# Kernel tuning notes

Hardware: AMD Instinct MI355X
Metric: run time of the kernel (lower is better)

Reference implementation:

```python
import jax, jax.numpy as jnp
import numpy as np

H, KVH, D = 32, 8, 128          # heads, kv heads, head dim
WINDOW = 512                     # sliding_window
NEG = -1e30


def _rotate_half(x):
    x1, x2 = jnp.split(x, 2, axis=-1)
    return jnp.concatenate([-x2, x1], axis=-1)


def setup_inputs() -> dict:
    key = jax.random.key(0)
    ks = jax.random.split(key, 6)
    B, S = 4, 1024
    T = B * S
    hidden = H * D  # 4096
    # RoPE tables [max_pos, head_dim]
    inv_freq = 1.0 / (10000.0 ** (jnp.arange(0, D, 2, dtype=jnp.float32) / D))
    freqs = jnp.outer(jnp.arange(S, dtype=jnp.float32), inv_freq)
    emb = jnp.concatenate([freqs, freqs], axis=-1)
    cos, sin = jnp.cos(emb), jnp.sin(emb)
    x = jax.random.normal(ks[0], (T, hidden), dtype=jnp.float32)
    pos = jnp.tile(jnp.arange(S, dtype=jnp.int64), B)            # positions restart per seq
    cu = jnp.arange(B + 1, dtype=jnp.int32) * S                  # uniform varlen offsets
    sc = 0.02
    Wq = jax.random.normal(ks[1], (hidden, H * D), jnp.float32) * sc
    Wk = jax.random.normal(ks[2], (hidden, KVH * D), jnp.float32) * sc
    Wv = jax.random.normal(ks[3], (hidden, KVH * D), jnp.float32) * sc
    Wo = jax.random.normal(ks[4], (H * D, hidden), jnp.float32) * sc
    return {"cos": cos, "sin": sin, "nz_hidden_states": x,
            "nz_position_ids": pos, "cu_seqlens": cu, "max_seqlen": S,
            "Wq": Wq, "Wk": Wk, "Wv": Wv, "Wo": Wo}


def reference(cos, sin, nz_hidden_states, nz_position_ids, cu_seqlens, max_seqlen,
              Wq, Wk, Wv, Wo):
    T = nz_hidden_states.shape[0]
    q = (nz_hidden_states @ Wq).reshape(T, H, D)
    k = (nz_hidden_states @ Wk).reshape(T, KVH, D)
    v = (nz_hidden_states @ Wv).reshape(T, KVH, D)
    # RoPE: gather by position, broadcast over head dim (unsqueeze(-2))
    c = cos[nz_position_ids][:, None, :]
    s = sin[nz_position_ids][:, None, :]
    q = q * c + _rotate_half(q) * s
    k = k * c + _rotate_half(k) * s
    # uniform varlen -> batch view [B, S, ...]
    B = cu_seqlens.shape[0] - 1
    S = T // B
    G = H // KVH  # query heads per kv head (GQA)
    qb = q.reshape(B, S, KVH, G, D)
    kb = k.reshape(B, S, KVH, D)
    vb = v.reshape(B, S, KVH, D)
    scores = jnp.einsum('bqhgd,bkhd->bhgqk', qb, kb) / jnp.sqrt(jnp.float32(D))
    i = jnp.arange(S)[:, None]
    j = jnp.arange(S)[None, :]
    mask = (j <= i) & (i - j <= WINDOW)  # causal + sliding window
    scores = jnp.where(mask, scores, NEG)
    p = jax.nn.softmax(scores, axis=-1)
    out = jnp.einsum('bhgqk,bkhd->bqhgd', p, vb).reshape(T, H * D)
    return out @ Wo
```

## Files before the change

### kernel.cpp

```cpp
#include <hip/hip_runtime.h>

typedef __bf16 bf16_t;
typedef __bf16 bf16x8 __attribute__((ext_vector_type(8)));
typedef __bf16 bf16x4 __attribute__((ext_vector_type(4)));
typedef float  f32x4  __attribute__((ext_vector_type(4)));
typedef float  f32x16 __attribute__((ext_vector_type(16)));
typedef unsigned int u32x4 __attribute__((ext_vector_type(4)));

#define N_HEADS 32
#define N_KVH   8
#define HEADDIM 128
#define WINDOW  512
#define NBATCH  4
#define SEQLEN  1024
#define NTOK    (NBATCH * SEQLEN)
#define HIDDEN  4096
#define QKVW    6144

__device__ __forceinline__ void llds16(const bf16_t* g, const bf16_t* l)
{
    __builtin_amdgcn_global_load_lds(
        (const __attribute__((address_space(1))) void*)g,
        (__attribute__((address_space(3))) void*)l, 16, 0, 0);
}

template<bool OUT_F32>
__global__ __launch_bounds__(512, 2)
void gemm256_kernel(const bf16_t* __restrict__ A, const bf16_t* __restrict__ Bt,
                    void* __restrict__ Cp, int M, int N, int K)
{
    __shared__ __align__(16) char lds[4 * 32768];
    const int tid  = threadIdx.x;
    const int w    = tid >> 6, lane = tid & 63;
    const int ntx  = N >> 8;
    const int nwg  = gridDim.x;
    const int cpx  = nwg >> 3;
    const int lin  = blockIdx.x;
    const int swz  = (nwg & 7) == 0 ? (lin & 7) * cpx + (lin >> 3) : lin;
    const int m0   = (swz / ntx) * 256;
    const int n0   = (swz % ntx) * 256;
    const int wm   = (w >> 2) * 128;
    const int wn   = (w & 3) * 64;
    const int fr   = lane & 15;
    const int kslot16 = (((lane >> 4) ^ ((lane >> 1) & 3)) << 4);
    const int srcblk  = (((tid & 3) ^ ((tid >> 3) & 3)) << 3);
    const int nk = K >> 5;

    f32x4 acc[8][4];
#pragma unroll
    for (int i = 0; i < 8; ++i)
#pragma unroll
        for (int j = 0; j < 4; ++j) {
            acc[i][j][0] = 0.f; acc[i][j][1] = 0.f;
            acc[i][j][2] = 0.f; acc[i][j][3] = 0.f;
        }

    const bf16_t* arow = A  + (size_t)(m0 + (tid >> 2)) * K + srcblk;
    const bf16_t* brow = Bt + (size_t)(n0 + (tid >> 2)) * K + srcblk;
    const size_t rowK128 = (size_t)128 * K;

    auto STAGE = [&](int tt) {
        char* dst = lds + (tt & 3) * 32768 + w * 1024;
        const int kt = tt << 5;
#pragma unroll
        for (int j = 0; j < 2; ++j)
            llds16(arow + j * rowK128 + kt, (const bf16_t*)(dst + j * 8192));
#pragma unroll
        for (int j = 0; j < 2; ++j)
            llds16(brow + j * rowK128 + kt, (const bf16_t*)(dst + 16384 + j * 8192));
    };

    STAGE(0); STAGE(1); STAGE(2);

    for (int t = 0; t < nk; ++t) {
        if (t < nk - 2)       asm volatile("s_waitcnt vmcnt(8)" ::: "memory");
        else if (t == nk - 2) asm volatile("s_waitcnt vmcnt(4)" ::: "memory");
        else                  asm volatile("s_waitcnt vmcnt(0)" ::: "memory");
        __builtin_amdgcn_sched_barrier(0);
        __builtin_amdgcn_s_barrier();
        __builtin_amdgcn_sched_barrier(0);

        const char* base = lds + (t & 3) * 32768;
        bf16x8 af[8], bfg[4];
#pragma unroll
        for (int mt = 0; mt < 8; ++mt)
            af[mt] = *(const bf16x8*)(base + ((wm + mt * 16 + fr) << 6) + kslot16);
#pragma unroll
        for (int nt = 0; nt < 4; ++nt)
            bfg[nt] = *(const bf16x8*)(base + 16384 + ((wn + nt * 16 + fr) << 6) + kslot16);

        if (t + 3 < nk) STAGE(t + 3);
        __builtin_amdgcn_s_setprio(1);
#pragma unroll
        for (int mt = 0; mt < 8; ++mt)
#pragma unroll
            for (int nt = 0; nt < 4; ++nt)
                acc[mt][nt] = __builtin_amdgcn_mfma_f32_16x16x32_bf16(
                    af[mt], bfg[nt], acc[mt][nt], 0, 0, 0);
        __builtin_amdgcn_s_setprio(0);
    }

    const int r0 = (lane >> 4) << 2;
#pragma unroll
    for (int mt = 0; mt < 8; ++mt)
#pragma unroll
        for (int nt = 0; nt < 4; ++nt)
#pragma unroll
            for (int r = 0; r < 4; ++r) {
                int row = m0 + wm + mt * 16 + r0 + r;
                int col = n0 + wn + nt * 16 + fr;
                if constexpr (OUT_F32)
                    ((float*)Cp)[(size_t)row * N + col] = acc[mt][nt][r];
                else
                    ((bf16_t*)Cp)[(size_t)row * N + col] = (bf16_t)acc[mt][nt][r];
            }
}

template<bool A_F32, bool OUT_F32>
__global__ __launch_bounds__(256)
void gemm_kernel(const void* __restrict__ Ap, const void* __restrict__ Bp,
                 void* __restrict__ Cp, int M, int N, int K)
{
    __shared__ bf16_t As[128 * 40];
    __shared__ bf16_t Bs[128 * 40];
    const int tid  = threadIdx.x;
    const int m0   = blockIdx.y * 128;
    const int n0   = blockIdx.x * 128;
    const int wave = tid >> 6, lane = tid & 63;
    const int wm   = (wave >> 1) * 64, wn = (wave & 1) * 64;
    const int fr   = lane & 15;
    const int koff = (lane >> 4) * 8;

    f32x4 acc[4][4];
#pragma unroll
    for (int i = 0; i < 4; ++i)
#pragma unroll
        for (int j = 0; j < 4; ++j) {
            acc[i][j][0] = 0.f; acc[i][j][1] = 0.f;
            acc[i][j][2] = 0.f; acc[i][j][3] = 0.f;
        }

    for (int kt = 0; kt < K; kt += 32) {
        __syncthreads();
        if constexpr (A_F32) {
            const float* A = (const float*)Ap;
#pragma unroll
            for (int i = 0; i < 4; ++i) {
                int lin = tid + i * 256;
                int row = lin >> 3;
                int kq  = (lin & 7) << 2;
                const float4 v = *(const float4*)(A + (size_t)(m0 + row) * K + kt + kq);
                bf16_t* d = &As[row * 40 + kq];
                d[0] = (bf16_t)v.x; d[1] = (bf16_t)v.y;
                d[2] = (bf16_t)v.z; d[3] = (bf16_t)v.w;
            }
        } else {
            const bf16_t* A = (const bf16_t*)Ap;
#pragma unroll
            for (int i = 0; i < 2; ++i) {
                int lin = tid + i * 256;
                int row = lin >> 2;
                int kq  = (lin & 3) << 3;
                *(bf16x8*)&As[row * 40 + kq] =
                    *(const bf16x8*)(A + (size_t)(m0 + row) * K + kt + kq);
            }
        }
        {
            const float* B = (const float*)Bp;
#pragma unroll
            for (int i = 0; i < 4; ++i) {
                int lin = tid + i * 256;
                int kr  = lin >> 5;
                int nc  = (lin & 31) << 2;
                const float4 v = *(const float4*)(B + (size_t)(kt + kr) * N + n0 + nc);
                Bs[(nc + 0) * 40 + kr] = (bf16_t)v.x;
                Bs[(nc + 1) * 40 + kr] = (bf16_t)v.y;
                Bs[(nc + 2) * 40 + kr] = (bf16_t)v.z;
                Bs[(nc + 3) * 40 + kr] = (bf16_t)v.w;
            }
        }
        __syncthreads();
        bf16x8 af[4], bfg[4];
#pragma unroll
        for (int mt = 0; mt < 4; ++mt)
            af[mt] = *(const bf16x8*)&As[(wm + mt * 16 + fr) * 40 + koff];
#pragma unroll
        for (int nt = 0; nt < 4; ++nt)
            bfg[nt] = *(const bf16x8*)&Bs[(wn + nt * 16 + fr) * 40 + koff];
#pragma unroll
        for (int mt = 0; mt < 4; ++mt)
#pragma unroll
            for (int nt = 0; nt < 4; ++nt)
                acc[mt][nt] = __builtin_amdgcn_mfma_f32_16x16x32_bf16(
                    af[mt], bfg[nt], acc[mt][nt], 0, 0, 0);
    }
    const int r0 = (lane >> 4) << 2;
#pragma unroll
    for (int mt = 0; mt < 4; ++mt)
#pragma unroll
        for (int nt = 0; nt < 4; ++nt)
#pragma unroll
            for (int r = 0; r < 4; ++r) {
                int row = m0 + wm + mt * 16 + r0 + r;
                int col = n0 + wn + nt * 16 + fr;
                if constexpr (OUT_F32)
                    ((float*)Cp)[(size_t)row * N + col] = acc[mt][nt][r];
                else
                    ((bf16_t*)Cp)[(size_t)row * N + col] = (bf16_t)acc[mt][nt][r];
            }
}

__global__ __launch_bounds__(256)
void f32_to_bf16_kernel(const float* __restrict__ in, bf16_t* __restrict__ out, int n8)
{
    int i = blockIdx.x * 256 + threadIdx.x;
    if (i >= n8) return;
    const float4 a = *(const float4*)(in + (size_t)i * 8);
    const float4 b = *(const float4*)(in + (size_t)i * 8 + 4);
    bf16x8 v;
    v[0] = (bf16_t)a.x; v[1] = (bf16_t)a.y; v[2] = (bf16_t)a.z; v[3] = (bf16_t)a.w;
    v[4] = (bf16_t)b.x; v[5] = (bf16_t)b.y; v[6] = (bf16_t)b.z; v[7] = (bf16_t)b.w;
    *(bf16x8*)(out + (size_t)i * 8) = v;
}

__global__ __launch_bounds__(256)
void wtrans_kernel(const float* __restrict__ W, bf16_t* __restrict__ Wt, int K, int N)
{
    __shared__ bf16_t tile[32][33];
    const int k0 = blockIdx.x * 32;
    const int n0 = blockIdx.y * 32;
    const int c  = threadIdx.x & 31, r0 = threadIdx.x >> 5;
#pragma unroll
    for (int i = 0; i < 4; ++i) {
        int r = r0 + i * 8;
        tile[r][c] = (bf16_t)W[(size_t)(k0 + r) * N + n0 + c];
    }
    __syncthreads();
#pragma unroll
    for (int i = 0; i < 4; ++i) {
        int r = r0 + i * 8;
        Wt[(size_t)(n0 + r) * K + k0 + c] = tile[c][r];
    }
}

__global__ __launch_bounds__(256)
void rope_kernel(bf16_t* __restrict__ qb, int qstr, bf16_t* __restrict__ kb, int kstr,
                 const float* __restrict__ cosT, const float* __restrict__ sinT)
{
    int lin  = blockIdx.x * 256 + threadIdx.x;
    int d    = lin & 63;
    int rest = lin >> 6;
    int head = rest % (N_HEADS + N_KVH);
    int t    = rest / (N_HEADS + N_KVH);
    if (t >= NTOK) return;
    int p = t & (SEQLEN - 1);
    float c = cosT[p * HEADDIM + d];
    float s = sinT[p * HEADDIM + d];
    bf16_t* ptr;
    float sc;
    if (head < N_HEADS) { ptr = qb + (size_t)t * qstr + head * HEADDIM; sc = 0.08838834764831845f; }
    else                { ptr = kb + (size_t)t * kstr + (head - N_HEADS) * HEADDIM; sc = 1.0f; }
    float x1 = (float)ptr[d], x2 = (float)ptr[d + 64];
    ptr[d]      = (bf16_t)((x1 * c - x2 * s) * sc);
    ptr[d + 64] = (bf16_t)((x2 * c + x1 * s) * sc);
}

__global__ __launch_bounds__(256)
void vtrans_kernel(const bf16_t* __restrict__ Vs, int vstr, bf16_t* __restrict__ Vt)
{
    __shared__ bf16_t tile[32][33];
    const int s0  = blockIdx.x * 32;
    const int d0  = blockIdx.y * 32;
    const int bk  = blockIdx.z;
    const int b   = bk >> 3, kvh = bk & 7;
    const int c   = threadIdx.x & 31, r0 = threadIdx.x >> 5;
    const bf16_t* src = Vs + (size_t)(b * SEQLEN + s0) * vstr + kvh * HEADDIM + d0;
#pragma unroll
    for (int i = 0; i < 4; ++i) {
        int r = r0 + i * 8;
        tile[r][c] = src[(size_t)r * vstr + c];
    }
    __syncthreads();
    bf16_t* dst = Vt + ((size_t)(b * N_KVH + kvh) * HEADDIM + d0) * SEQLEN + s0;
#pragma unroll
    for (int i = 0; i < 4; ++i) {
        int dr = r0 + i * 8;
        dst[(size_t)dr * SEQLEN + c] = tile[c][dr];
    }
}

__device__ __forceinline__ unsigned int pk2(float a, float b)
{
    unsigned short x = __builtin_bit_cast(unsigned short, (bf16_t)a);
    unsigned short y = __builtin_bit_cast(unsigned short, (bf16_t)b);
    return ((unsigned int)y << 16) | (unsigned int)x;
}
__device__ __forceinline__ void swap32(unsigned int& a, unsigned int& b)
{
    asm volatile("v_permlane32_swap_b32 %0, %1" : "+v"(a), "+v"(b));
}

__device__ __forceinline__ void stage_kv(const bf16_t* __restrict__ Kb, int kstr,
                                         const bf16_t* __restrict__ Vt,
                                         char* ldsb, int bb, int kvh, int kb,
                                         int w, int i)
{
#pragma unroll
    for (int j = 0; j < 2; ++j) {
        int row = w * 8 + j * 4 + (i >> 4);
        const bf16_t* src = Kb + (size_t)(bb * SEQLEN + kb + row) * kstr + kvh * HEADDIM
                          + (((i & 15) ^ (row & 7)) << 3);
        llds16(src, (const bf16_t*)(ldsb + (w * 8 + j * 4) * 256));
    }
#pragma unroll
    for (int j = 0; j < 2; ++j) {
        int d = w * 16 + j * 8 + (i >> 3);
        const bf16_t* src = Vt + ((size_t)((bb * N_KVH + kvh) * HEADDIM + d)) * SEQLEN + kb
                          + (((i & 7) ^ (d & 7)) << 3);
        llds16(src, (const bf16_t*)(ldsb + 16384 + (w * 16 + j * 8) * 128));
    }
}

__global__ __launch_bounds__(512, 2)
void attn32_kernel(const bf16_t* __restrict__ Qb, const bf16_t* __restrict__ Kb,
                   const bf16_t* __restrict__ Vt, bf16_t* __restrict__ Ob,
                   int qstr, int kstr)
{
    __shared__ __align__(16) char lds[65536];
    const int tid = threadIdx.x, w = tid >> 6, i = tid & 63;
    const int la = i & 31, hi = i >> 5;
    const int qt = blockIdx.x, kvh = blockIdx.y, bb = blockIdx.z;
    const int Q0 = qt * 64;
    const int h  = kvh * 4 + (w >> 1);
    const int qw = Q0 + 32 * (w & 1);
    const int KL = Q0 >= WINDOW ? Q0 - WINDOW : 0;
    const int nt = (Q0 - KL) / 64 + 1;
    const int iq = qw + la;

    const bf16_t* qp = Qb + (size_t)(bb * SEQLEN + iq) * qstr + h * HEADDIM + 8 * hi;
    bf16x8 qf[8];
#pragma unroll
    for (int c = 0; c < 8; ++c) qf[c] = *(const bf16x8*)(qp + c * 16);

    f32x16 oacc[4];
#pragma unroll
    for (int d = 0; d < 4; ++d)
#pragma unroll
        for (int r = 0; r < 16; ++r) oacc[d][r] = 0.f;
    float mrow = -1e30f, lsum = 0.f;

    stage_kv(Kb, kstr, Vt, lds, bb, kvh, KL, w, i);

    const int cswz = (la & 7) << 4;

    for (int t = 0; t < nt; ++t) {
        asm volatile("s_waitcnt vmcnt(0) lgkmcnt(0)" ::: "memory");
        __builtin_amdgcn_sched_barrier(0);
        __syncthreads();
        if (t + 1 < nt)
            stage_kv(Kb, kstr, Vt, lds + ((t + 1) & 1) * 32768, bb, kvh, KL + (t + 1) * 64, w, i);
        const char* KsB = lds + (t & 1) * 32768;
        const char* VsB = KsB + 16384;
        const int kb = KL + t * 64;

        f32x16 s0, s1;
#pragma unroll
        for (int r = 0; r < 16; ++r) { s0[r] = 0.f; s1[r] = 0.f; }
        __builtin_amdgcn_s_setprio(1);
#pragma unroll
        for (int c = 0; c < 8; ++c) {
            bf16x8 k0 = *(const bf16x8*)(KsB + la * 256        + ((c * 32 + 16 * hi) ^ cswz));
            bf16x8 k1 = *(const bf16x8*)(KsB + (la + 32) * 256 + ((c * 32 + 16 * hi) ^ cswz));
            s0 = __builtin_amdgcn_mfma_f32_32x32x16_bf16(k0, qf[c], s0, 0, 0, 0);
            s1 = __builtin_amdgcn_mfma_f32_32x32x16_bf16(k1, qf[c], s1, 0, 0, 0);
        }
        __builtin_amdgcn_s_setprio(0);

        const bool interior = (kb + 63 <= qw) && (kb >= qw - (WINDOW - 31));
        if (!interior) {
#pragma unroll
            for (int r = 0; r < 16; ++r) {
                int j0 = kb + (r & 3) + 8 * (r >> 2) + 4 * hi;
                int j1 = j0 + 32;
                if (!(j0 <= iq && iq - j0 <= WINDOW)) s0[r] = -1e30f;
                if (!(j1 <= iq && iq - j1 <= WINDOW)) s1[r] = -1e30f;
            }
        }

        float mt = fmaxf(s0[0], s1[0]);
#pragma unroll
        for (int r = 1; r < 16; ++r) mt = fmaxf(mt, fmaxf(s0[r], s1[r]));
        mt = fmaxf(mt, __shfl_xor(mt, 32, 64));
        float mnew = fmaxf(mrow, mt);
        float corr = __expf(mrow - mnew);
        float ps = 0.f;
#pragma unroll
        for (int r = 0; r < 16; ++r) {
            s0[r] = __expf(s0[r] - mnew);
            s1[r] = __expf(s1[r] - mnew);
            ps += s0[r] + s1[r];
        }
        ps += __shfl_xor(ps, 32, 64);
        lsum = lsum * corr + ps;
        mrow = mnew;
#pragma unroll
        for (int d = 0; d < 4; ++d)
#pragma unroll
            for (int r = 0; r < 16; ++r) oacc[d][r] *= corr;

        bf16x8 pa[4];
        {
            unsigned int w0 = pk2(s0[0], s0[1]),  w1 = pk2(s0[2], s0[3]);
            unsigned int w2 = pk2(s0[4], s0[5]),  w3 = pk2(s0[6], s0[7]);
            swap32(w0, w2); swap32(w1, w3);
            u32x4 u; u[0] = w0; u[1] = w1; u[2] = w2; u[3] = w3;
            pa[0] = __builtin_bit_cast(bf16x8, u);
            w0 = pk2(s0[8], s0[9]);   w1 = pk2(s0[10], s0[11]);
            w2 = pk2(s0[12], s0[13]); w3 = pk2(s0[14], s0[15]);
            swap32(w0, w2); swap32(w1, w3);
            u[0] = w0; u[1] = w1; u[2] = w2; u[3] = w3;
            pa[1] = __builtin_bit_cast(bf16x8, u);
            w0 = pk2(s1[0], s1[1]);  w1 = pk2(s1[2], s1[3]);
            w2 = pk2(s1[4], s1[5]);  w3 = pk2(s1[6], s1[7]);
            swap32(w0, w2); swap32(w1, w3);
            u[0] = w0; u[1] = w1; u[2] = w2; u[3] = w3;
            pa[2] = __builtin_bit_cast(bf16x8, u);
            w0 = pk2(s1[8], s1[9]);   w1 = pk2(s1[10], s1[11]);
            w2 = pk2(s1[12], s1[13]); w3 = pk2(s1[14], s1[15]);
            swap32(w0, w2); swap32(w1, w3);
            u[0] = w0; u[1] = w1; u[2] = w2; u[3] = w3;
            pa[3] = __builtin_bit_cast(bf16x8, u);
        }

        __builtin_amdgcn_s_setprio(1);
#pragma unroll
        for (int d = 0; d < 4; ++d) {
            const char* vrow = VsB + (d * 32 + la) * 128;
#pragma unroll
            for (int ks = 0; ks < 4; ++ks) {
                bf16x8 vf = *(const bf16x8*)(vrow + ((ks * 32 + 16 * hi) ^ cswz));
                oacc[d] = __builtin_amdgcn_mfma_f32_32x32x16_bf16(vf, pa[ks], oacc[d], 0, 0, 0);
            }
        }
        __builtin_amdgcn_s_setprio(0);
    }

    float rn = 1.f / lsum;
    bf16_t* orow = Ob + ((size_t)((bb * SEQLEN + iq) * N_HEADS + h)) * HEADDIM;
#pragma unroll
    for (int d = 0; d < 4; ++d)
#pragma unroll
        for (int g = 0; g < 4; ++g) {
            bf16x4 v;
            v[0] = (bf16_t)(oacc[d][4 * g + 0] * rn);
            v[1] = (bf16_t)(oacc[d][4 * g + 1] * rn);
            v[2] = (bf16_t)(oacc[d][4 * g + 2] * rn);
            v[3] = (bf16_t)(oacc[d][4 * g + 3] * rn);
            *(bf16x4*)(orow + d * 32 + 8 * g + 4 * hi) = v;
        }
}

extern "C" void kernel_launch(void* const* d_in, const int* in_sizes, int n_in,
                              void* d_out, int out_size, void* d_ws, size_t ws_size,
                              hipStream_t stream)
{
    const float* cosT = (const float*)d_in[0];
    const float* sinT = (const float*)d_in[1];
    const float* x    = (const float*)d_in[2];
    const float* Wq   = (const float*)d_in[6];
    const float* Wk   = (const float*)d_in[7];
    const float* Wv   = (const float*)d_in[8];
    const float* Wo   = (const float*)d_in[9];
    float* out = (float*)d_out;
    char* ws = (char*)d_ws;
    const size_t MB = 1024ull * 1024ull;

    if (ws_size >= 136 * MB) {
        bf16_t* Xb    = (bf16_t*)(ws);
        bf16_t* Wqkvt = (bf16_t*)(ws + 32 * MB);
        bf16_t* QKVb  = (bf16_t*)(ws + 80 * MB);
        bf16_t* Vt    = (bf16_t*)(ws + 128 * MB);
        bf16_t* Ob    = Xb;

        f32_to_bf16_kernel<<<(NTOK * HIDDEN / 8 + 255) / 256, 256, 0, stream>>>(x, Xb, NTOK * HIDDEN / 8);
        wtrans_kernel<<<dim3(HIDDEN/32, HIDDEN/32), 256, 0, stream>>>(Wq, Wqkvt, HIDDEN, HIDDEN);
        wtrans_kernel<<<dim3(HIDDEN/32, 1024/32), 256, 0, stream>>>(Wk, Wqkvt + (size_t)4096 * HIDDEN, HIDDEN, 1024);
        wtrans_kernel<<<dim3(HIDDEN/32, 1024/32), 256, 0, stream>>>(Wv, Wqkvt + (size_t)5120 * HIDDEN, HIDDEN, 1024);
        gemm256_kernel<false><<<dim3((NTOK/256) * (QKVW/256)), 512, 0, stream>>>(Xb, Wqkvt, QKVb, NTOK, QKVW, HIDDEN);
        rope_kernel<<<(NTOK * (N_HEADS + N_KVH) * 64) / 256, 256, 0, stream>>>(QKVb, QKVW, QKVb + 4096, QKVW, cosT, sinT);
        vtrans_kernel<<<dim3(SEQLEN/32, HEADDIM/32, NBATCH * N_KVH), 256, 0, stream>>>(QKVb + 5120, QKVW, Vt);
        attn32_kernel<<<dim3(SEQLEN/64, N_KVH, NBATCH), 512, 0, stream>>>(QKVb, QKVb + 4096, Vt, Ob, QKVW, QKVW);
        wtrans_kernel<<<dim3(HIDDEN/32, HIDDEN/32), 256, 0, stream>>>(Wo, Wqkvt, HIDDEN, HIDDEN);
        gemm256_kernel<true><<<dim3((NTOK/256) * (HIDDEN/256)), 512, 0, stream>>>(Ob, Wqkvt, out, NTOK, HIDDEN, HIDDEN);
    } else {
        bf16_t* Qb = (bf16_t*)(ws);
        bf16_t* Kb = (bf16_t*)(ws + 32 * MB);
        bf16_t* Vb = (bf16_t*)(ws + 40 * MB);
        bf16_t* Vt = (bf16_t*)(ws + 48 * MB);
        bf16_t* Ob = (bf16_t*)(ws + 56 * MB);
        gemm_kernel<true, false><<<dim3(32, 32), 256, 0, stream>>>(x, Wq, Qb, NTOK, HIDDEN, HIDDEN);
        gemm_kernel<true, false><<<dim3(8, 32), 256, 0, stream>>>(x, Wk, Kb, NTOK, 1024, HIDDEN);
        gemm_kernel<true, false><<<dim3(8, 32), 256, 0, stream>>>(x, Wv, Vb, NTOK, 1024, HIDDEN);
        rope_kernel<<<(NTOK * (N_HEADS + N_KVH) * 64) / 256, 256, 0, stream>>>(Qb, HIDDEN, Kb, 1024, cosT, sinT);
        vtrans_kernel<<<dim3(SEQLEN/32, HEADDIM/32, NBATCH * N_KVH), 256, 0, stream>>>(Vb, 1024, Vt);
        attn32_kernel<<<dim3(SEQLEN/64, N_KVH, NBATCH), 512, 0, stream>>>(Qb, Kb, Vt, Ob, HIDDEN, 1024);
        gemm_kernel<false, true><<<dim3(32, 32), 256, 0, stream>>>(Ob, Wo, out, NTOK, HIDDEN, HIDDEN);
    }
}
```

Baseline: 504.9 us.

## Add 256x128-tile GEMM with triple-buffered LDS for QKV projection

Adds a new GEMM kernel with a 256x128 output tile, BK=32, three LDS buffers (72KB) and launch bounds allowing four workgroups per CU, and uses it for the fused QKV projection instead of the 256x256 kernel. This doubles the number of workgroups (16x48=768), aiming at better CU occupancy and load balance on the 256-CU device, with deeper prefetch hiding memory latency. The cost is lower operand reuse per tile, more global traffic for A, and register pressure from the launch-bounds limit.

```diff
diff --git a/kernel.cpp b/kernel.cpp
--- a/kernel.cpp
+++ b/kernel.cpp
@@ -22,6 +22,99 @@
     __builtin_amdgcn_global_load_lds(
         (const __attribute__((address_space(1))) void*)g,
         (__attribute__((address_space(3))) void*)l, 16, 0, 0);
+}
+
+template<bool OUT_F32>
+__global__ __launch_bounds__(512, 4)
+void gemm_dual_kernel(const bf16_t* __restrict__ A, const bf16_t* __restrict__ Bt,
+                      void* __restrict__ Cp, int M, int N, int K)
+{
+    __shared__ __align__(16) char lds[3 * 24576];
+    const int tid  = threadIdx.x;
+    const int w    = tid >> 6, lane = tid & 63;
+    const int ntx  = N >> 7;
+    const int nwg  = gridDim.x;
+    const int cpx  = nwg >> 3;
+    const int lin  = blockIdx.x;
+    const int swz  = (nwg & 7) == 0 ? (lin & 7) * cpx + (lin >> 3) : lin;
+    const int m0   = (swz / ntx) * 256;
+    const int n0   = (swz % ntx) * 128;
+    const int wm   = (w >> 1) * 64;
+    const int wn   = (w & 1) * 64;
+    const int fr   = lane & 15;
+    const int kslot16 = (((lane >> 4) ^ ((lane >> 1) & 3)) << 4);
+    const int srcblk  = (((tid & 3) ^ ((tid >> 3) & 3)) << 3);
+    const int nk = K >> 5;
+
+    f32x4 acc[4][4];
+#pragma unroll
+    for (int i = 0; i < 4; ++i)
+#pragma unroll
+        for (int j = 0; j < 4; ++j) {
+            acc[i][j][0] = 0.f; acc[i][j][1] = 0.f;
+            acc[i][j][2] = 0.f; acc[i][j][3] = 0.f;
+        }
+
+    const bf16_t* arow = A  + (size_t)(m0 + (tid >> 2)) * K + srcblk;
+    const bf16_t* brow = Bt + (size_t)(n0 + (tid >> 2)) * K + srcblk;
+    const size_t rowK128 = (size_t)128 * K;
+
+    auto STAGE = [&](int tt, int buf) {
+        char* dst = lds + buf * 24576 + w * 1024;
+        const int kt = tt << 5;
+        llds16(arow + kt,           (const bf16_t*)(dst));
+        llds16(arow + rowK128 + kt, (const bf16_t*)(dst + 8192));
+        llds16(brow + kt,           (const bf16_t*)(dst + 16384));
+    };
+
+    STAGE(0, 0); STAGE(1, 1);
+
+    int cur = 0;
+    for (int t = 0; t < nk; ++t) {
+        if (t + 1 < nk) asm volatile("s_waitcnt vmcnt(3)" ::: "memory");
+        else            asm volatile("s_waitcnt vmcnt(0)" ::: "memory");
+        __builtin_amdgcn_sched_barrier(0);
+        __builtin_amdgcn_s_barrier();
+        __builtin_amdgcn_sched_barrier(0);
+
+        const char* base = lds + cur * 24576;
+        bf16x8 af[4], bfg[4];
+#pragma unroll
+        for (int mt = 0; mt < 4; ++mt)
+            af[mt] = *(const bf16x8*)(base + ((wm + mt * 16 + fr) << 6) + kslot16);
+#pragma unroll
+        for (int nt = 0; nt < 4; ++nt)
+            bfg[nt] = *(const bf16x8*)(base + 16384 + ((wn + nt * 16 + fr) << 6) + kslot16);
+
+        if (t + 2 < nk) {
+            int nb = cur + 2; if (nb >= 3) nb -= 3;
+            STAGE(t + 2, nb);
+        }
+        __builtin_amdgcn_s_setprio(1);
+#pragma unroll
+        for (int mt = 0; mt < 4; ++mt)
+#pragma unroll
+            for (int nt = 0; nt < 4; ++nt)
+                acc[mt][nt] = __builtin_amdgcn_mfma_f32_16x16x32_bf16(
+                    af[mt], bfg[nt], acc[mt][nt], 0, 0, 0);
+        __builtin_amdgcn_s_setprio(0);
+        ++cur; if (cur == 3) cur = 0;
+    }
+
+    const int r0 = (lane >> 4) << 2;
+#pragma unroll
+    for (int mt = 0; mt < 4; ++mt)
+#pragma unroll
+        for (int nt = 0; nt < 4; ++nt)
+#pragma unroll
+            for (int r = 0; r < 4; ++r) {
+                int row = m0 + wm + mt * 16 + r0 + r;
+                int col = n0 + wn + nt * 16 + fr;
+                if constexpr (OUT_F32)
+                    ((float*)Cp)[(size_t)row * N + col] = acc[mt][nt][r];
+                else
+                    ((bf16_t*)Cp)[(size_t)row * N + col] = (bf16_t)acc[mt][nt][r];
+            }
 }
 
 template<bool OUT_F32>
@@ -486,7 +579,7 @@
         wtrans_kernel<<<dim3(HIDDEN/32, HIDDEN/32), 256, 0, stream>>>(Wq, Wqkvt, HIDDEN, HIDDEN);
         wtrans_kernel<<<dim3(HIDDEN/32, 1024/32), 256, 0, stream>>>(Wk, Wqkvt + (size_t)4096 * HIDDEN, HIDDEN, 1024);
         wtrans_kernel<<<dim3(HIDDEN/32, 1024/32), 256, 0, stream>>>(Wv, Wqkvt + (size_t)5120 * HIDDEN, HIDDEN, 1024);
-        gemm256_kernel<false><<<dim3((NTOK/256) * (QKVW/256)), 512, 0, stream>>>(Xb, Wqkvt, QKVb, NTOK, QKVW, HIDDEN);
+        gemm_dual_kernel<false><<<dim3((NTOK/256) * (QKVW/128)), 512, 0, stream>>>(Xb, Wqkvt, QKVb, NTOK, QKVW, HIDDEN);
         rope_kernel<<<(NTOK * (N_HEADS + N_KVH) * 64) / 256, 256, 0, stream>>>(QKVb, QKVW, QKVb + 4096, QKVW, cosT, sinT);
         vtrans_kernel<<<dim3(SEQLEN/32, HEADDIM/32, NBATCH * N_KVH), 256, 0, stream>>>(QKVb + 5120, QKVW, Vt);
         attn32_kernel<<<dim3(SEQLEN/64, N_KVH, NBATCH), 512, 0, stream>>>(QKVb, QKVb + 4096, Vt, Ob, QKVW, QKVW);
```

New measurement: 491.9 us. 2.6% less time.
